# Performance work log

Measured on AMD Instinct MI355X. Metric: run time of the kernel, lower is better.

The kernel has to match this reference:

```python
import jax, jax.numpy as jnp
import numpy as np

N_TOKENS = 32768
INPUT_DIM = 1024
HIDDEN_DIM = 256
NUM_EXPERTS = 64
TOP_K = 2


def setup_inputs() -> dict:
    key = jax.random.key(0)
    kx, k1, k2, kb1, kb2 = jax.random.split(key, 5)
    # torch nn.Linear init scale ~ U(-1/sqrt(fan_in), 1/sqrt(fan_in)); use small normals
    x = jax.random.normal(kx, (N_TOKENS, INPUT_DIM), dtype=jnp.float32)
    w1 = jax.random.normal(k1, (HIDDEN_DIM, INPUT_DIM), dtype=jnp.float32) / np.sqrt(INPUT_DIM)
    b1 = jax.random.normal(kb1, (HIDDEN_DIM,), dtype=jnp.float32) * 0.01
    w2 = jax.random.normal(k2, (NUM_EXPERTS, HIDDEN_DIM), dtype=jnp.float32) / np.sqrt(HIDDEN_DIM)
    b2 = jax.random.normal(kb2, (NUM_EXPERTS,), dtype=jnp.float32) * 0.01
    return {"x": x, "w1": w1, "b1": b1, "w2": w2, "b2": b2}


def reference(x, w1, b1, w2, b2):
    # logits = Linear -> ReLU -> Linear
    h = jax.nn.relu(jnp.einsum("nd,hd->nh", x, w1) + b1)       # [N, hidden]
    logits = jnp.einsum("nh,eh->ne", h, w2) + b2               # [N, experts]
    top_k_logits, top_k_indices = jax.lax.top_k(logits, TOP_K)  # [N, k]
    top_k_gates = jax.nn.softmax(top_k_logits, axis=-1)
    return top_k_indices, top_k_gates
```

## Files before the change

### kernel.cpp

```cpp
#include <hip/hip_runtime.h>
#include <math.h>

#define N_TOK 32768
#define IN_DIM 1024
#define HID 256
#define NE 64

union SMem {
    struct { float Xs[32][32]; float Ws[32][256]; } a;
    float Hs[32][260];
};

__global__ __launch_bounds__(128, 2)
void moe_gate(const float* __restrict__ x,  const float* __restrict__ w1,
              const float* __restrict__ b1, const float* __restrict__ w2,
              const float* __restrict__ b2, float* __restrict__ out)
{
    __shared__ SMem sm;

    const int tid = threadIdx.x;
    const int tg  = tid >> 5;
    const int hg  = tid & 31;
    const int t0  = blockIdx.x * 32;

    float acc[8][8];
    #pragma unroll
    for (int i = 0; i < 8; ++i)
        #pragma unroll
        for (int j = 0; j < 8; ++j) acc[i][j] = 0.f;

    #pragma unroll 1
    for (int c = 0; c < 32; ++c) {
        const int k0 = c * 32;
        #pragma unroll
        for (int r = 0; r < 2; ++r) {
            int slot = tid + 128 * r;
            int t = slot >> 3, kq = (slot & 7) * 4;
            float4 v = *(const float4*)(x + (size_t)(t0 + t) * IN_DIM + k0 + kq);
            int col = (((t >> 2) ^ (kq >> 2)) << 2) | (t & 3);
            sm.a.Xs[kq + 0][col] = v.x;
            sm.a.Xs[kq + 1][col] = v.y;
            sm.a.Xs[kq + 2][col] = v.z;
            sm.a.Xs[kq + 3][col] = v.w;
        }
        #pragma unroll
        for (int r = 0; r < 16; ++r) {
            int slot = tid + 128 * r;
            int hh = slot >> 3, kq = (slot & 7) * 4;
            float4 v = *(const float4*)(w1 + (size_t)hh * IN_DIM + k0 + kq);
            int col = (((hh >> 2) ^ (kq >> 2)) << 2) | (hh & 3);
            sm.a.Ws[kq + 0][col] = v.x;
            sm.a.Ws[kq + 1][col] = v.y;
            sm.a.Ws[kq + 2][col] = v.z;
            sm.a.Ws[kq + 3][col] = v.w;
        }
        __syncthreads();

        #pragma unroll
        for (int m = 0; m < 8; ++m) {
            const float* xb0 = &sm.a.Xs[0][(((tg * 2)     ^ m) << 2)];
            const float* xb1 = &sm.a.Xs[0][(((tg * 2 + 1) ^ m) << 2)];
            const float* wb0 = &sm.a.Ws[0][(( hg ^ m)         << 2)];
            const float* wb1 = &sm.a.Ws[0][((((hg ^ m) + 32)) << 2)];
            #pragma unroll
            for (int kk = 0; kk < 4; ++kk) {
                int k = m * 4 + kk;
                float4 xv0 = *(const float4*)(xb0 + k * 32);
                float4 xv1 = *(const float4*)(xb1 + k * 32);
                float4 wv0 = *(const float4*)(wb0 + k * 256);
                float4 wv1 = *(const float4*)(wb1 + k * 256);
                float xv[8] = {xv0.x, xv0.y, xv0.z, xv0.w, xv1.x, xv1.y, xv1.z, xv1.w};
                float wv[8] = {wv0.x, wv0.y, wv0.z, wv0.w, wv1.x, wv1.y, wv1.z, wv1.w};
                #pragma unroll
                for (int i = 0; i < 8; ++i)
                    #pragma unroll
                    for (int j = 0; j < 8; ++j)
                        acc[i][j] = fmaf(xv[i], wv[j], acc[i][j]);
            }
        }
        __syncthreads();
    }

    {
        float4 bb0 = *(const float4*)(b1 + hg * 4);
        float4 bb1 = *(const float4*)(b1 + 128 + hg * 4);
        float bias1[8] = {bb0.x, bb0.y, bb0.z, bb0.w, bb1.x, bb1.y, bb1.z, bb1.w};
        #pragma unroll
        for (int i = 0; i < 8; ++i)
            #pragma unroll
            for (int j = 0; j < 8; ++j)
                acc[i][j] = fmaxf(acc[i][j] + bias1[j], 0.f);
    }

    #pragma unroll
    for (int i = 0; i < 8; ++i) {
        *(float4*)&sm.Hs[tg * 8 + i][hg * 4] =
            make_float4(acc[i][0], acc[i][1], acc[i][2], acc[i][3]);
        *(float4*)&sm.Hs[tg * 8 + i][128 + hg * 4] =
            make_float4(acc[i][4], acc[i][5], acc[i][6], acc[i][7]);
    }
    __syncthreads();

    const int tp = tid >> 4;
    const int e4 = tid & 15;

    const float* hp[4] = { &sm.Hs[tp * 4 + 0][0], &sm.Hs[tp * 4 + 1][0],
                           &sm.Hs[tp * 4 + 2][0], &sm.Hs[tp * 4 + 3][0] };
    const float* w2p = w2 + (size_t)(e4 * 4) * HID;

    float acc2[4][4];
    #pragma unroll
    for (int i = 0; i < 4; ++i)
        #pragma unroll
        for (int j = 0; j < 4; ++j) acc2[i][j] = 0.f;

    #pragma unroll 2
    for (int k4 = 0; k4 < 64; ++k4) {
        const int k = k4 * 4;
        float hvv[4][4], evv[4][4];
        #pragma unroll
        for (int i = 0; i < 4; ++i)
            *(float4*)&hvv[i][0] = *(const float4*)(hp[i] + k);
        #pragma unroll
        for (int j = 0; j < 4; ++j)
            *(float4*)&evv[j][0] = *(const float4*)(w2p + (size_t)j * HID + k);
        #pragma unroll
        for (int d = 0; d < 4; ++d)
            #pragma unroll
            for (int i = 0; i < 4; ++i)
                #pragma unroll
                for (int j = 0; j < 4; ++j)
                    acc2[i][j] = fmaf(hvv[i][d], evv[j][d], acc2[i][j]);
    }

    float4 b2v = *(const float4*)(b2 + e4 * 4);
    #pragma unroll
    for (int i = 0; i < 4; ++i) {
        float v[4] = {acc2[i][0] + b2v.x, acc2[i][1] + b2v.y,
                      acc2[i][2] + b2v.z, acc2[i][3] + b2v.w};
        float m1 = -INFINITY, m2 = -INFINITY;
        int i1 = 0, i2 = 0;
        #pragma unroll
        for (int j = 0; j < 4; ++j) {
            int e = e4 * 4 + j;
            if (v[j] > m1)      { m2 = m1; i2 = i1; m1 = v[j]; i1 = e; }
            else if (v[j] > m2) { m2 = v[j]; i2 = e; }
        }
        #pragma unroll
        for (int off = 1; off < 16; off <<= 1) {
            float om1 = __shfl_xor(m1, off);
            int   oi1 = __shfl_xor(i1, off);
            float om2 = __shfl_xor(m2, off);
            int   oi2 = __shfl_xor(i2, off);
            bool bwin = (om1 > m1) || (om1 == m1 && oi1 < i1);
            float c1v = bwin ? om1 : m1;  int c1i = bwin ? oi1 : i1;
            float lv  = bwin ? m1  : om1; int li  = bwin ? i1  : oi1;
            float w2v = bwin ? om2 : m2;  int w2i = bwin ? oi2 : i2;
            bool s = (lv > w2v) || (lv == w2v && li < w2i);
            m1 = c1v; i1 = c1i;
            m2 = s ? lv : w2v; i2 = s ? li : w2i;
        }
        if (e4 == 0) {
            float ex  = expf(m2 - m1);
            float inv = 1.f / (1.f + ex);
            int gt = t0 + tp * 4 + i;
            out[(size_t)gt * 2 + 0] = (float)i1;
            out[(size_t)gt * 2 + 1] = (float)i2;
            out[(size_t)2 * N_TOK + (size_t)gt * 2 + 0] = inv;
            out[(size_t)2 * N_TOK + (size_t)gt * 2 + 1] = ex * inv;
        }
    }
}

extern "C" void kernel_launch(void* const* d_in, const int* in_sizes, int n_in,
                              void* d_out, int out_size, void* d_ws, size_t ws_size,
                              hipStream_t stream) {
    const float* x  = (const float*)d_in[0];
    const float* w1 = (const float*)d_in[1];
    const float* b1 = (const float*)d_in[2];
    const float* w2 = (const float*)d_in[3];
    const float* b2 = (const float*)d_in[4];
    float* out = (float*)d_out;

    moe_gate<<<N_TOK / 32, 128, 0, stream>>>(x, w1, b1, w2, b2, out);
}
```

Before: 412.4 us.

## Pre-transpose w1, DMA W tiles into LDS, stream X tiles through registers

A small kernel now transposes w1 into the workspace on every call, so each W1 k-slice is a contiguous block. The main kernel copies that block straight into LDS with global_load_lds instead of doing register loads and scattered swizzled stores. X is no longer staged in LDS: each thread reads its 8 token rows as float2 pairs straight from global memory, prefetching the next pair while it does the FMAs. This removes the LDS traffic and swizzle arithmetic for X, but adds broadcast-heavy, poorly coalesced global loads of X, an extra launch, and an unpadded Hs buffer that may add LDS bank conflicts in the second GEMM.

Result: slower. 461.8 us (+12.0%).

```diff
diff --git a/kernel.cpp b/kernel.cpp
--- a/kernel.cpp
+++ b/kernel.cpp
@@ -6,13 +6,42 @@
 #define HID 256
 #define NE 64
 
+__global__ __launch_bounds__(256)
+void transpose_w1(const float* __restrict__ w1, float* __restrict__ w1t)
+{
+    __shared__ float tile[32][33];
+    const int k0 = blockIdx.x * 32;
+    const int h0 = blockIdx.y * 32;
+    const int j  = threadIdx.x & 31;
+    const int i0 = threadIdx.x >> 5;
+    #pragma unroll
+    for (int r = 0; r < 4; ++r) {
+        int i = i0 + r * 8;
+        tile[i][j] = w1[(size_t)(h0 + i) * IN_DIM + k0 + j];
+    }
+    __syncthreads();
+    #pragma unroll
+    for (int r = 0; r < 4; ++r) {
+        int i = i0 + r * 8;
+        w1t[(size_t)(k0 + i) * HID + h0 + j] = tile[j][i];
+    }
+}
+
+__device__ __forceinline__ void gload_lds16(const float* g, float* l)
+{
+    __builtin_amdgcn_global_load_lds(
+        (const __attribute__((address_space(1))) void*)g,
+        (__attribute__((address_space(3))) void*)l,
+        16, 0, 0);
+}
+
 union SMem {
-    struct { float Xs[32][32]; float Ws[32][256]; } a;
-    float Hs[32][260];
+    float Ws[32][256];
+    float Hs[32][256];
 };
 
 __global__ __launch_bounds__(128, 2)
-void moe_gate(const float* __restrict__ x,  const float* __restrict__ w1,
+void moe_gate(const float* __restrict__ x,  const float* __restrict__ w1t,
               const float* __restrict__ b1, const float* __restrict__ w2,
               const float* __restrict__ b2, float* __restrict__ out)
 {
@@ -23,6 +52,9 @@
     const int hg  = tid & 31;
     const int t0  = blockIdx.x * 32;
 
+    const float* xb   = x + (size_t)(t0 + tg * 8) * IN_DIM;
+    const float* wrow = &sm.Ws[0][hg * 4];
+
     float acc[8][8];
     #pragma unroll
     for (int i = 0; i < 8; ++i)
@@ -32,50 +64,87 @@
     #pragma unroll 1
     for (int c = 0; c < 32; ++c) {
         const int k0 = c * 32;
-        #pragma unroll
-        for (int r = 0; r < 2; ++r) {
-            int slot = tid + 128 * r;
-            int t = slot >> 3, kq = (slot & 7) * 4;
-            float4 v = *(const float4*)(x + (size_t)(t0 + t) * IN_DIM + k0 + kq);
-            int col = (((t >> 2) ^ (kq >> 2)) << 2) | (t & 3);
-            sm.a.Xs[kq + 0][col] = v.x;
-            sm.a.Xs[kq + 1][col] = v.y;
-            sm.a.Xs[kq + 2][col] = v.z;
-            sm.a.Xs[kq + 3][col] = v.w;
-        }
+
         #pragma unroll
         for (int r = 0; r < 16; ++r) {
             int slot = tid + 128 * r;
-            int hh = slot >> 3, kq = (slot & 7) * 4;
-            float4 v = *(const float4*)(w1 + (size_t)hh * IN_DIM + k0 + kq);
-            int col = (((hh >> 2) ^ (kq >> 2)) << 2) | (hh & 3);
-            sm.a.Ws[kq + 0][col] = v.x;
-            sm.a.Ws[kq + 1][col] = v.y;
-            sm.a.Ws[kq + 2][col] = v.z;
-            sm.a.Ws[kq + 3][col] = v.w;
-        }
+            gload_lds16(w1t + (size_t)k0 * HID + slot * 4, &sm.Ws[0][0] + slot * 4);
+        }
+
+        float2 xA[8], xB[8];
+        #pragma unroll
+        for (int t = 0; t < 8; ++t)
+            xA[t] = *(const float2*)(xb + (size_t)t * IN_DIM + k0);
+        #pragma unroll
+        for (int t = 0; t < 8; ++t)
+            xB[t] = *(const float2*)(xb + (size_t)t * IN_DIM + k0 + 2);
+
         __syncthreads();
 
         #pragma unroll
-        for (int m = 0; m < 8; ++m) {
-            const float* xb0 = &sm.a.Xs[0][(((tg * 2)     ^ m) << 2)];
-            const float* xb1 = &sm.a.Xs[0][(((tg * 2 + 1) ^ m) << 2)];
-            const float* wb0 = &sm.a.Ws[0][(( hg ^ m)         << 2)];
-            const float* wb1 = &sm.a.Ws[0][((((hg ^ m) + 32)) << 2)];
-            #pragma unroll
-            for (int kk = 0; kk < 4; ++kk) {
-                int k = m * 4 + kk;
-                float4 xv0 = *(const float4*)(xb0 + k * 32);
-                float4 xv1 = *(const float4*)(xb1 + k * 32);
-                float4 wv0 = *(const float4*)(wb0 + k * 256);
-                float4 wv1 = *(const float4*)(wb1 + k * 256);
-                float xv[8] = {xv0.x, xv0.y, xv0.z, xv0.w, xv1.x, xv1.y, xv1.z, xv1.w};
-                float wv[8] = {wv0.x, wv0.y, wv0.z, wv0.w, wv1.x, wv1.y, wv1.z, wv1.w};
+        for (int g = 0; g < 8; ++g) {
+            const int k = g * 4;
+            float4 w00 = *(const float4*)(wrow + (k + 0) * 256);
+            float4 w01 = *(const float4*)(wrow + (k + 0) * 256 + 128);
+            float4 w10 = *(const float4*)(wrow + (k + 1) * 256);
+            float4 w11 = *(const float4*)(wrow + (k + 1) * 256 + 128);
+            #pragma unroll
+            for (int t = 0; t < 8; ++t) {
+                acc[t][0] = fmaf(xA[t].x, w00.x, acc[t][0]);
+                acc[t][1] = fmaf(xA[t].x, w00.y, acc[t][1]);
+                acc[t][2] = fmaf(xA[t].x, w00.z, acc[t][2]);
+                acc[t][3] = fmaf(xA[t].x, w00.w, acc[t][3]);
+                acc[t][4] = fmaf(xA[t].x, w01.x, acc[t][4]);
+                acc[t][5] = fmaf(xA[t].x, w01.y, acc[t][5]);
+                acc[t][6] = fmaf(xA[t].x, w01.z, acc[t][6]);
+                acc[t][7] = fmaf(xA[t].x, w01.w, acc[t][7]);
+            }
+            #pragma unroll
+            for (int t = 0; t < 8; ++t) {
+                acc[t][0] = fmaf(xA[t].y, w10.x, acc[t][0]);
+                acc[t][1] = fmaf(xA[t].y, w10.y, acc[t][1]);
+                acc[t][2] = fmaf(xA[t].y, w10.z, acc[t][2]);
+                acc[t][3] = fmaf(xA[t].y, w10.w, acc[t][3]);
+                acc[t][4] = fmaf(xA[t].y, w11.x, acc[t][4]);
+                acc[t][5] = fmaf(xA[t].y, w11.y, acc[t][5]);
+                acc[t][6] = fmaf(xA[t].y, w11.z, acc[t][6]);
+                acc[t][7] = fmaf(xA[t].y, w11.w, acc[t][7]);
+            }
+            if (g < 7) {
                 #pragma unroll
-                for (int i = 0; i < 8; ++i)
-                    #pragma unroll
-                    for (int j = 0; j < 8; ++j)
-                        acc[i][j] = fmaf(xv[i], wv[j], acc[i][j]);
+                for (int t = 0; t < 8; ++t)
+                    xA[t] = *(const float2*)(xb + (size_t)t * IN_DIM + k0 + k + 4);
+            }
+            float4 w20 = *(const float4*)(wrow + (k + 2) * 256);
+            float4 w21 = *(const float4*)(wrow + (k + 2) * 256 + 128);
+            float4 w30 = *(const float4*)(wrow + (k + 3) * 256);
+            float4 w31 = *(const float4*)(wrow + (k + 3) * 256 + 128);
+            #pragma unroll
+            for (int t = 0; t < 8; ++t) {
+                acc[t][0] = fmaf(xB[t].x, w20.x, acc[t][0]);
+                acc[t][1] = fmaf(xB[t].x, w20.y, acc[t][1]);
+                acc[t][2] = fmaf(xB[t].x, w20.z, acc[t][2]);
+                acc[t][3] = fmaf(xB[t].x, w20.w, acc[t][3]);
+                acc[t][4] = fmaf(xB[t].x, w21.x, acc[t][4]);
+                acc[t][5] = fmaf(xB[t].x, w21.y, acc[t][5]);
+                acc[t][6] = fmaf(xB[t].x, w21.z, acc[t][6]);
+                acc[t][7] = fmaf(xB[t].x, w21.w, acc[t][7]);
+            }
+            #pragma unroll
+            for (int t = 0; t < 8; ++t) {
+                acc[t][0] = fmaf(xB[t].y, w30.x, acc[t][0]);
+                acc[t][1] = fmaf(xB[t].y, w30.y, acc[t][1]);
+                acc[t][2] = fmaf(xB[t].y, w30.z, acc[t][2]);
+                acc[t][3] = fmaf(xB[t].y, w30.w, acc[t][3]);
+                acc[t][4] = fmaf(xB[t].y, w31.x, acc[t][4]);
+                acc[t][5] = fmaf(xB[t].y, w31.y, acc[t][5]);
+                acc[t][6] = fmaf(xB[t].y, w31.z, acc[t][6]);
+                acc[t][7] = fmaf(xB[t].y, w31.w, acc[t][7]);
+            }
+            if (g < 7) {
+                #pragma unroll
+                for (int t = 0; t < 8; ++t)
+                    xB[t] = *(const float2*)(xb + (size_t)t * IN_DIM + k0 + k + 6);
             }
         }
         __syncthreads();
@@ -181,6 +250,8 @@
     const float* w2 = (const float*)d_in[3];
     const float* b2 = (const float*)d_in[4];
     float* out = (float*)d_out;
-
-    moe_gate<<<N_TOK / 32, 128, 0, stream>>>(x, w1, b1, w2, b2, out);
-}
+    float* w1t = (float*)d_ws;
+
+    transpose_w1<<<dim3(32, 8), 256, 0, stream>>>(w1, w1t);
+    moe_gate<<<N_TOK / 32, 128, 0, stream>>>(x, w1t, b1, w2, b2, out);
+}
```
